# Kernel tuning notes

Hardware: AMD Instinct MI355X
Metric: run time of the kernel (lower is better)

The kernel has to match this reference:

```python
import math
import jax, jax.numpy as jnp
import numpy as np

B, H, S, D = 2, 16, 2048, 64


def setup_inputs() -> dict:
    key = jax.random.key(0)
    kq, kk, kv = jax.random.split(key, 3)
    query = jax.random.normal(kq, (B, H, S, D), dtype=jnp.float32)
    k = jax.random.normal(kk, (B, H, S, D), dtype=jnp.float32)
    value = jax.random.normal(kv, (B, H, S, D), dtype=jnp.float32)
    # causal mask: True = keep, broadcasts over batch and heads
    mask = jnp.tril(jnp.ones((S, S), dtype=bool))
    return {"query": query, "key": k, "value": value, "mask": mask}


def reference(query, key, value, mask):
    d_k = query.shape[-1]
    scale = 1.0 / math.sqrt(d_k)
    # (..., s1, s2) materialized scores, as in the original module
    scores = jnp.einsum("bhqd,bhkd->bhqk", query, key) * scale
    scores = jnp.where(mask, scores, -jnp.inf)
    # stable softmax = exp(x - max) / sum, same math as the torch softmax helper
    attn = jax.nn.softmax(scores, axis=-1)
    return jnp.einsum("bhqk,bhkd->bhqd", attn, value)
```

## Files before the change

### kernel.cpp

```cpp
#include <hip/hip_runtime.h>
#include <hip/hip_bf16.h>


typedef __attribute__((ext_vector_type(8))) short  s8v;
typedef __attribute__((ext_vector_type(4))) float  f4v;
typedef __attribute__((ext_vector_type(4))) unsigned int u4v;

#define SEQ 2048
#define DH  64
#define BHN 32
#define CSC 0.18033688f

#if __has_builtin(__builtin_amdgcn_exp2f)
#define EXP2(x) __builtin_amdgcn_exp2f(x)
#else
#define EXP2(x) exp2f(x)
#endif

__device__ __forceinline__ unsigned short f2bf(float x) {
  union { float f; unsigned int u; } v; v.f = x;
  return (unsigned short)((v.u + 0x7fffu + ((v.u >> 16) & 1u)) >> 16);
}
__device__ __forceinline__ float bf2f(unsigned short x) {
  union { unsigned int u; float f; } v; v.u = ((unsigned int)x) << 16;
  return v.f;
}
__device__ __forceinline__ int pack_bf2(float a, float b) {
  union { __hip_bfloat162 h; int i; } u;
  u.h = __float22bfloat162_rn(make_float2(a, b));
  return u.i;
}
__device__ __forceinline__ bool probe_is_f32(const unsigned short* p) {
  const unsigned e = (p[threadIdx.x & 63] >> 7) & 0xFFu;
  return __ballot(e >= 0x89u) != 0ULL;
}
__device__ __forceinline__ s8v cvt8(const float* p) {
  float4 a = *(const float4*)p;
  float4 b = *(const float4*)(p + 4);
  s8v r;
  r[0] = (short)f2bf(a.x); r[1] = (short)f2bf(a.y);
  r[2] = (short)f2bf(a.z); r[3] = (short)f2bf(a.w);
  r[4] = (short)f2bf(b.x); r[5] = (short)f2bf(b.y);
  r[6] = (short)f2bf(b.z); r[7] = (short)f2bf(b.w);
  return r;
}
__device__ __forceinline__ s8v cvt8s(const float* p, float s) {
  float4 a = *(const float4*)p;
  float4 b = *(const float4*)(p + 4);
  s8v r;
  r[0] = (short)f2bf(a.x * s); r[1] = (short)f2bf(a.y * s);
  r[2] = (short)f2bf(a.z * s); r[3] = (short)f2bf(a.w * s);
  r[4] = (short)f2bf(b.x * s); r[5] = (short)f2bf(b.y * s);
  r[6] = (short)f2bf(b.z * s); r[7] = (short)f2bf(b.w * s);
  return r;
}
__device__ __forceinline__ void gld16(const void* g, void* l) {
  __builtin_amdgcn_global_load_lds(
      (const __attribute__((address_space(1))) void*)g,
      (__attribute__((address_space(3))) void*)l, 16, 0, 0);
}

__global__ __launch_bounds__(256) void prep_kernel(
    const void* __restrict__ Kv, const void* __restrict__ Vv,
    unsigned short* __restrict__ Kbf, unsigned short* __restrict__ Vt) {
  const int bh = blockIdx.y;
  const int s0 = blockIdx.x * 64;
  const int t  = threadIdx.x;
  if (blockIdx.z == 0) {
    const unsigned short* K16 = (const unsigned short*)Kv;
    const float*          KF  = (const float*)Kv;
    const bool isF32 = probe_is_f32(K16);
    const int sr  = t >> 2;
    const int cb0 = (t & 3) * 32;
    const int xs  = (sr & 7) << 4;
    const size_t src = ((size_t)(bh * SEQ + s0 + sr)) * DH + (t & 3) * 16;
    s8v a0, a1;
    if (!isF32) { a0 = *(const s8v*)(K16 + src); a1 = *(const s8v*)(K16 + src + 8); }
    else        { a0 = cvt8(KF + src);           a1 = cvt8(KF + src + 8); }
    char* rowp = (char*)Kbf + ((size_t)(bh * SEQ + s0 + sr)) * 128;
    *(s8v*)(rowp + (cb0 ^ xs))        = a0;
    *(s8v*)(rowp + ((cb0 + 16) ^ xs)) = a1;
  } else {
    __shared__ __align__(16) unsigned short T[64][72];
    const unsigned short* V16 = (const unsigned short*)Vv;
    const float*          VF  = (const float*)Vv;
    const bool isF32 = probe_is_f32(V16);
    {
      const int sr = t >> 2, c0 = (t & 3) * 16;
      const size_t base = ((size_t)(bh * SEQ + s0 + sr)) * DH + c0;
      s8v a0, a1;
      if (!isF32) { a0 = *(const s8v*)(V16 + base); a1 = *(const s8v*)(V16 + base + 8); }
      else        { a0 = cvt8(VF + base);           a1 = cvt8(VF + base + 8); }
      *(s8v*)&T[sr][c0]     = a0;
      *(s8v*)&T[sr][c0 + 8] = a1;
    }
    __syncthreads();
    {
      const int d  = t & 63;
      const int hs = t >> 6;
      const int xs = (d & 7) << 4;
      char* rowp = (char*)Vt + (size_t)bh * SEQ * 128 + (size_t)s0 * 128
                 + (size_t)d * 128;
#pragma unroll
      for (int cc = 0; cc < 2; ++cc) {
        const int c  = hs * 2 + cc;
        const int kA = (c >> 2) * 32 + (c & 3) * 4;
        unsigned int wb[4];
        wb[0] = (unsigned int)T[kA + 0][d]  | ((unsigned int)T[kA + 1][d]  << 16);
        wb[1] = (unsigned int)T[kA + 2][d]  | ((unsigned int)T[kA + 3][d]  << 16);
        wb[2] = (unsigned int)T[kA + 16][d] | ((unsigned int)T[kA + 17][d] << 16);
        wb[3] = (unsigned int)T[kA + 18][d] | ((unsigned int)T[kA + 19][d] << 16);
        u4v q = { wb[0], wb[1], wb[2], wb[3] };
        *(u4v*)(rowp + ((c * 16) ^ xs)) = q;
      }
    }
  }
}

__global__ __launch_bounds__(128, 2) void attn_kernel(
    const void* __restrict__ Qv, const unsigned short* __restrict__ Kbf,
    const unsigned short* __restrict__ Vt, void* __restrict__ Outv) {
  __shared__ __align__(16) char Lds[2][16384];

  const unsigned short* Q16 = (const unsigned short*)Qv;
  const float*          QF  = (const float*)Qv;
  const bool isF32 = probe_is_f32(Q16);

  const int blk = blockIdx.x;
  const int bh  = (blk & 7) * 4 + ((blk >> 3) & 3);
  const int a   = (blk >> 5) & 7;
  const int bsl = blk >> 8;
  const int qb  = (bsl == 0) ? (7 - a) : (bsl == 1) ? (8 + a)
                : (bsl == 2) ? (23 - a) : (24 + a);

  const int tid  = threadIdx.x;
  const int w    = tid >> 6;
  const int lane = tid & 63;
  const int quad = lane >> 4;
  const int c16  = lane & 15;
  const int q0   = qb * 64 + w * 32;

  const size_t bh_off = (size_t)bh * SEQ * DH;

  s8v aq[2][2];
#pragma unroll
  for (int h = 0; h < 2; ++h)
#pragma unroll
    for (int kc = 0; kc < 2; ++kc) {
      const size_t idx = bh_off + (size_t)(q0 + h * 16 + c16) * DH + kc * 32 + quad * 8;
      if (isF32) aq[h][kc] = cvt8s(QF + idx, CSC);
      else {
        s8v aa = *(const s8v*)(Q16 + idx);
#pragma unroll
        for (int t = 0; t < 8; ++t)
          aa[t] = (short)f2bf(bf2f((unsigned short)aa[t]) * CSC);
        aq[h][kc] = aa;
      }
    }

  f4v o[2][4];
  float l[2] = {0.f, 0.f};
#pragma unroll
  for (int h = 0; h < 2; ++h)
#pragma unroll
    for (int i = 0; i < 4; ++i) { f4v z = {0.f, 0.f, 0.f, 0.f}; o[h][i] = z; }

  const int ntiles = qb + 1;

  const int xorl = (c16 & 7) << 4;
  const int fc0  = (quad * 16) ^ xorl;
  const int fc1  = (64 + quad * 16) ^ xorl;
  const int frow = c16 * 128;

  const unsigned short* Kg = Kbf + bh_off + (size_t)lane * 8;
  const unsigned short* Vg = Vt  + bh_off + (size_t)lane * 8;

  auto stage = [&](int tile, int buf) {
    if (w == 0) {
      const unsigned short* g = Kg + (size_t)tile * 4096;
      char* lp = &Lds[buf][0];
#pragma unroll
      for (int j = 0; j < 8; ++j) gld16(g + j * 512, lp + j * 1024);
    } else {
      const unsigned short* g = Vg + (size_t)tile * 4096;
      char* lp = &Lds[buf][8192];
#pragma unroll
      for (int j = 0; j < 8; ++j) gld16(g + j * 512, lp + j * 1024);
    }
  };

  stage(0, 0);
  __syncthreads();

  for (int kt = 0; kt < ntiles; ++kt) {
    const int cb = kt & 1, nb = cb ^ 1;
    if (kt + 1 < ntiles) stage(kt + 1, nb);

    const char* Kl = &Lds[cb][0];
    const char* Vl = &Lds[cb][8192];
    s8v kb[4][2], vb[4][2];
#pragma unroll
    for (int nt = 0; nt < 4; ++nt) {
      kb[nt][0] = *(const s8v*)(Kl + frow + nt * 2048 + fc0);
      kb[nt][1] = *(const s8v*)(Kl + frow + nt * 2048 + fc1);
      vb[nt][0] = *(const s8v*)(Vl + frow + nt * 2048 + fc0);
      vb[nt][1] = *(const s8v*)(Vl + frow + nt * 2048 + fc1);
    }

    __builtin_amdgcn_s_setprio(1);
    float p[2][4][4];
#pragma unroll
    for (int h = 0; h < 2; ++h)
#pragma unroll
      for (int nt = 0; nt < 4; ++nt) {
        f4v acc = {0.f, 0.f, 0.f, 0.f};
        acc = __builtin_amdgcn_mfma_f32_16x16x32_bf16(kb[nt][0], aq[h][0], acc, 0, 0, 0);
        acc = __builtin_amdgcn_mfma_f32_16x16x32_bf16(kb[nt][1], aq[h][1], acc, 0, 0, 0);
#pragma unroll
        for (int r = 0; r < 4; ++r) p[h][nt][r] = EXP2(acc[r]);
      }
    if (kt * 64 + 63 > q0) {
#pragma unroll
      for (int h = 0; h < 2; ++h) {
        const int qmk = q0 + h * 16 + c16 - kt * 64 - quad * 4;
#pragma unroll
        for (int nt = 0; nt < 4; ++nt)
#pragma unroll
          for (int r = 0; r < 4; ++r)
            if (nt * 16 + r > qmk) p[h][nt][r] = 0.f;
      }
    }
#pragma unroll
    for (int h = 0; h < 2; ++h) {
      float s = 0.f;
#pragma unroll
      for (int nt = 0; nt < 4; ++nt)
        s += (p[h][nt][0] + p[h][nt][1]) + (p[h][nt][2] + p[h][nt][3]);
      l[h] += s;
#pragma unroll
      for (int kc = 0; kc < 2; ++kc) {
        union { int d[4]; s8v v; } u;
        u.d[0] = pack_bf2(p[h][2 * kc][0],     p[h][2 * kc][1]);
        u.d[1] = pack_bf2(p[h][2 * kc][2],     p[h][2 * kc][3]);
        u.d[2] = pack_bf2(p[h][2 * kc + 1][0], p[h][2 * kc + 1][1]);
        u.d[3] = pack_bf2(p[h][2 * kc + 1][2], p[h][2 * kc + 1][3]);
#pragma unroll
        for (int dt = 0; dt < 4; ++dt)
          o[h][dt] = __builtin_amdgcn_mfma_f32_16x16x32_bf16(u.v, vb[dt][kc], o[h][dt], 0, 0, 0);
      }
    }
    __builtin_amdgcn_s_setprio(0);

    __syncthreads();
  }

#pragma unroll
  for (int h = 0; h < 2; ++h) {
    float lv = l[h];
    lv += __shfl_xor(lv, 16);
    lv += __shfl_xor(lv, 32);
    union { float f; int i; } lu; lu.f = lv;
    float invr[4];
#pragma unroll
    for (int rr = 0; rr < 4; ++rr) {
      union { int i; float f; } tf;
      tf.i = __builtin_amdgcn_ds_bpermute(4 * (quad * 4 + rr), lu.i);
      invr[rr] = 1.0f / tf.f;
    }
    if (isF32) {
      float* OF = (float*)Outv;
#pragma unroll
      for (int rr = 0; rr < 4; ++rr) {
        const size_t rb = bh_off + (size_t)(q0 + h * 16 + quad * 4 + rr) * DH + c16;
#pragma unroll
        for (int dt = 0; dt < 4; ++dt)
          OF[rb + dt * 16] = o[h][dt][rr] * invr[rr];
      }
    } else {
      unsigned short* O16 = (unsigned short*)Outv;
#pragma unroll
      for (int rr = 0; rr < 4; ++rr) {
        const size_t rb = bh_off + (size_t)(q0 + h * 16 + quad * 4 + rr) * DH + c16;
#pragma unroll
        for (int dt = 0; dt < 4; ++dt)
          O16[rb + dt * 16] = f2bf(o[h][dt][rr] * invr[rr]);
      }
    }
  }
}

extern "C" void kernel_launch(void* const* d_in, const int* in_sizes, int n_in,
                              void* d_out, int out_size, void* d_ws, size_t ws_size,
                              hipStream_t stream) {
  const void* Q = d_in[0];
  const void* K = d_in[1];
  const void* V = d_in[2];
  unsigned short* Kbf = (unsigned short*)d_ws;
  unsigned short* Vt  = Kbf + (size_t)BHN * SEQ * DH;

  dim3 g1(SEQ / 64, BHN, 2);
  prep_kernel<<<g1, 256, 0, stream>>>(K, V, Kbf, Vt);
  attn_kernel<<<dim3(1024), 128, 0, stream>>>(Q, Kbf, Vt, d_out);
}
```

Before: 138.5 us.

## Split KV tiles across waves with per-wave pipelines and LDS merge

Rather than two waves each owning 32 query rows and sharing one KV tile per iteration, each wave now handles all 64 query rows and takes alternate KV tiles. Each wave runs its own double-buffered LDS pipeline with explicit vmcnt/lgkmcnt waits, so the per-tile __syncthreads is gone. The two partial outputs and row sums are merged through LDS at the end. Block ordering becomes a plain largest-first order. The cost is twice the accumulator registers, 64KB of LDS per block (which may limit occupancy), and possible imbalance when the tile count is odd.

Result: slower. 154.0 us (+11.2%).

```diff
diff --git a/kernel.cpp b/kernel.cpp
--- a/kernel.cpp
+++ b/kernel.cpp
@@ -120,7 +120,7 @@
 __global__ __launch_bounds__(128, 2) void attn_kernel(
     const void* __restrict__ Qv, const unsigned short* __restrict__ Kbf,
     const unsigned short* __restrict__ Vt, void* __restrict__ Outv) {
-  __shared__ __align__(16) char Lds[2][16384];
+  __shared__ __align__(16) char Lds[65536];
 
   const unsigned short* Q16 = (const unsigned short*)Qv;
   const float*          QF  = (const float*)Qv;
@@ -128,23 +128,23 @@
 
   const int blk = blockIdx.x;
   const int bh  = (blk & 7) * 4 + ((blk >> 3) & 3);
-  const int a   = (blk >> 5) & 7;
-  const int bsl = blk >> 8;
-  const int qb  = (bsl == 0) ? (7 - a) : (bsl == 1) ? (8 + a)
-                : (bsl == 2) ? (23 - a) : (24 + a);
+  const int qb  = 31 - (blk >> 5);
 
   const int tid  = threadIdx.x;
   const int w    = tid >> 6;
   const int lane = tid & 63;
   const int quad = lane >> 4;
   const int c16  = lane & 15;
-  const int q0   = qb * 64 + w * 32;
+  const int q0   = qb * 64;
+
+  const int ntiles = qb + 1;
+  const int nw = (ntiles - w + 1) >> 1;
 
   const size_t bh_off = (size_t)bh * SEQ * DH;
 
-  s8v aq[2][2];
-#pragma unroll
-  for (int h = 0; h < 2; ++h)
+  s8v aq[4][2];
+#pragma unroll
+  for (int h = 0; h < 4; ++h)
 #pragma unroll
     for (int kc = 0; kc < 2; ++kc) {
       const size_t idx = bh_off + (size_t)(q0 + h * 16 + c16) * DH + kc * 32 + quad * 8;
@@ -158,14 +158,12 @@
       }
     }
 
-  f4v o[2][4];
-  float l[2] = {0.f, 0.f};
-#pragma unroll
-  for (int h = 0; h < 2; ++h)
+  f4v o[4][4];
+  float l[4] = {0.f, 0.f, 0.f, 0.f};
+#pragma unroll
+  for (int h = 0; h < 4; ++h)
 #pragma unroll
     for (int i = 0; i < 4; ++i) { f4v z = {0.f, 0.f, 0.f, 0.f}; o[h][i] = z; }
-
-  const int ntiles = qb + 1;
 
   const int xorl = (c16 & 7) << 4;
   const int fc0  = (quad * 16) ^ xorl;
@@ -175,115 +173,153 @@
   const unsigned short* Kg = Kbf + bh_off + (size_t)lane * 8;
   const unsigned short* Vg = Vt  + bh_off + (size_t)lane * 8;
 
+  char* LdsW = &Lds[w * 32768];
+
   auto stage = [&](int tile, int buf) {
-    if (w == 0) {
-      const unsigned short* g = Kg + (size_t)tile * 4096;
-      char* lp = &Lds[buf][0];
-#pragma unroll
-      for (int j = 0; j < 8; ++j) gld16(g + j * 512, lp + j * 1024);
+    const unsigned short* gk = Kg + (size_t)tile * 4096;
+    const unsigned short* gv = Vg + (size_t)tile * 4096;
+    char* lk = LdsW + buf * 16384;
+    char* lv = lk + 8192;
+#pragma unroll
+    for (int j = 0; j < 8; ++j) gld16(gk + j * 512, lk + j * 1024);
+#pragma unroll
+    for (int j = 0; j < 8; ++j) gld16(gv + j * 512, lv + j * 1024);
+  };
+
+  if (nw > 0) {
+    stage(w, 0);
+    if (nw > 1) {
+      stage(w + 2, 1);
+      asm volatile("s_waitcnt vmcnt(16)" ::: "memory");
     } else {
-      const unsigned short* g = Vg + (size_t)tile * 4096;
-      char* lp = &Lds[buf][8192];
-#pragma unroll
-      for (int j = 0; j < 8; ++j) gld16(g + j * 512, lp + j * 1024);
-    }
-  };
-
-  stage(0, 0);
-  __syncthreads();
-
-  for (int kt = 0; kt < ntiles; ++kt) {
-    const int cb = kt & 1, nb = cb ^ 1;
-    if (kt + 1 < ntiles) stage(kt + 1, nb);
-
-    const char* Kl = &Lds[cb][0];
-    const char* Vl = &Lds[cb][8192];
-    s8v kb[4][2], vb[4][2];
-#pragma unroll
-    for (int nt = 0; nt < 4; ++nt) {
-      kb[nt][0] = *(const s8v*)(Kl + frow + nt * 2048 + fc0);
-      kb[nt][1] = *(const s8v*)(Kl + frow + nt * 2048 + fc1);
-      vb[nt][0] = *(const s8v*)(Vl + frow + nt * 2048 + fc0);
-      vb[nt][1] = *(const s8v*)(Vl + frow + nt * 2048 + fc1);
-    }
-
-    __builtin_amdgcn_s_setprio(1);
-    float p[2][4][4];
-#pragma unroll
-    for (int h = 0; h < 2; ++h)
+      asm volatile("s_waitcnt vmcnt(0)" ::: "memory");
+    }
+    __builtin_amdgcn_sched_barrier(0);
+
+    for (int j = 0; j < nw; ++j) {
+      const int kt = w + 2 * j;
+      const int cb = j & 1;
+
+      const char* Kl = LdsW + cb * 16384;
+      const char* Vl = Kl + 8192;
+      s8v kb[4][2], vb[4][2];
 #pragma unroll
       for (int nt = 0; nt < 4; ++nt) {
-        f4v acc = {0.f, 0.f, 0.f, 0.f};
-        acc = __builtin_amdgcn_mfma_f32_16x16x32_bf16(kb[nt][0], aq[h][0], acc, 0, 0, 0);
-        acc = __builtin_amdgcn_mfma_f32_16x16x32_bf16(kb[nt][1], aq[h][1], acc, 0, 0, 0);
-#pragma unroll
-        for (int r = 0; r < 4; ++r) p[h][nt][r] = EXP2(acc[r]);
-      }
-    if (kt * 64 + 63 > q0) {
-#pragma unroll
-      for (int h = 0; h < 2; ++h) {
-        const int qmk = q0 + h * 16 + c16 - kt * 64 - quad * 4;
+        kb[nt][0] = *(const s8v*)(Kl + frow + nt * 2048 + fc0);
+        kb[nt][1] = *(const s8v*)(Kl + frow + nt * 2048 + fc1);
+        vb[nt][0] = *(const s8v*)(Vl + frow + nt * 2048 + fc0);
+        vb[nt][1] = *(const s8v*)(Vl + frow + nt * 2048 + fc1);
+      }
+      asm volatile("s_waitcnt lgkmcnt(0)" ::: "memory");
+      __builtin_amdgcn_sched_barrier(0);
+
+      if (j + 2 < nw) stage(w + 2 * (j + 2), cb);
+
+      const bool diag = (kt == qb);
+      __builtin_amdgcn_s_setprio(1);
+#pragma unroll
+      for (int h = 0; h < 4; ++h) {
+        float p[4][4];
+#pragma unroll
+        for (int nt = 0; nt < 4; ++nt) {
+          f4v acc = {0.f, 0.f, 0.f, 0.f};
+          acc = __builtin_amdgcn_mfma_f32_16x16x32_bf16(kb[nt][0], aq[h][0], acc, 0, 0, 0);
+          acc = __builtin_amdgcn_mfma_f32_16x16x32_bf16(kb[nt][1], aq[h][1], acc, 0, 0, 0);
+#pragma unroll
+          for (int r = 0; r < 4; ++r) p[nt][r] = EXP2(acc[r]);
+        }
+        if (diag) {
+          const int qmk = q0 + h * 16 + c16 - kt * 64 - quad * 4;
+#pragma unroll
+          for (int nt = 0; nt < 4; ++nt)
+#pragma unroll
+            for (int r = 0; r < 4; ++r)
+              if (nt * 16 + r > qmk) p[nt][r] = 0.f;
+        }
+        float s = 0.f;
 #pragma unroll
         for (int nt = 0; nt < 4; ++nt)
-#pragma unroll
-          for (int r = 0; r < 4; ++r)
-            if (nt * 16 + r > qmk) p[h][nt][r] = 0.f;
-      }
-    }
-#pragma unroll
-    for (int h = 0; h < 2; ++h) {
-      float s = 0.f;
-#pragma unroll
-      for (int nt = 0; nt < 4; ++nt)
-        s += (p[h][nt][0] + p[h][nt][1]) + (p[h][nt][2] + p[h][nt][3]);
-      l[h] += s;
-#pragma unroll
-      for (int kc = 0; kc < 2; ++kc) {
-        union { int d[4]; s8v v; } u;
-        u.d[0] = pack_bf2(p[h][2 * kc][0],     p[h][2 * kc][1]);
-        u.d[1] = pack_bf2(p[h][2 * kc][2],     p[h][2 * kc][3]);
-        u.d[2] = pack_bf2(p[h][2 * kc + 1][0], p[h][2 * kc + 1][1]);
-        u.d[3] = pack_bf2(p[h][2 * kc + 1][2], p[h][2 * kc + 1][3]);
-#pragma unroll
-        for (int dt = 0; dt < 4; ++dt)
-          o[h][dt] = __builtin_amdgcn_mfma_f32_16x16x32_bf16(u.v, vb[dt][kc], o[h][dt], 0, 0, 0);
-      }
-    }
-    __builtin_amdgcn_s_setprio(0);
-
-    __syncthreads();
-  }
-
-#pragma unroll
-  for (int h = 0; h < 2; ++h) {
+          s += (p[nt][0] + p[nt][1]) + (p[nt][2] + p[nt][3]);
+        l[h] += s;
+#pragma unroll
+        for (int kc = 0; kc < 2; ++kc) {
+          union { int d[4]; s8v v; } u;
+          u.d[0] = pack_bf2(p[2 * kc][0],     p[2 * kc][1]);
+          u.d[1] = pack_bf2(p[2 * kc][2],     p[2 * kc][3]);
+          u.d[2] = pack_bf2(p[2 * kc + 1][0], p[2 * kc + 1][1]);
+          u.d[3] = pack_bf2(p[2 * kc + 1][2], p[2 * kc + 1][3]);
+#pragma unroll
+          for (int dt = 0; dt < 4; ++dt)
+            o[h][dt] = __builtin_amdgcn_mfma_f32_16x16x32_bf16(u.v, vb[dt][kc], o[h][dt], 0, 0, 0);
+        }
+      }
+      __builtin_amdgcn_s_setprio(0);
+
+      if (j + 1 < nw) {
+        if (j + 2 < nw) asm volatile("s_waitcnt vmcnt(16)" ::: "memory");
+        else            asm volatile("s_waitcnt vmcnt(0)"  ::: "memory");
+        __builtin_amdgcn_sched_barrier(0);
+      }
+    }
+  }
+
+  f4v lpack;
+#pragma unroll
+  for (int h = 0; h < 4; ++h) {
     float lv = l[h];
     lv += __shfl_xor(lv, 16);
     lv += __shfl_xor(lv, 32);
-    union { float f; int i; } lu; lu.f = lv;
-    float invr[4];
-#pragma unroll
-    for (int rr = 0; rr < 4; ++rr) {
-      union { int i; float f; } tf;
-      tf.i = __builtin_amdgcn_ds_bpermute(4 * (quad * 4 + rr), lu.i);
-      invr[rr] = 1.0f / tf.f;
-    }
-    if (isF32) {
-      float* OF = (float*)Outv;
+    lpack[h] = lv;
+  }
+  {
+    char* C = LdsW;
+#pragma unroll
+    for (int h = 0; h < 4; ++h)
+#pragma unroll
+      for (int dt = 0; dt < 4; ++dt)
+        *(f4v*)(C + lane * 256 + (h * 4 + dt) * 16) = o[h][dt];
+    *(f4v*)(C + 16384 + lane * 16) = lpack;
+  }
+  __syncthreads();
+  {
+    const char* P = &Lds[(1 - w) * 32768];
+    const f4v pl = *(const f4v*)(P + 16384 + lane * 16);
+#pragma unroll
+    for (int hh = 0; hh < 2; ++hh) {
+      const int h = 2 * w + hh;
+      const float ltot = lpack[h] + pl[h];
+      union { float f; int i; } lu; lu.f = ltot;
+      float invr[4];
 #pragma unroll
       for (int rr = 0; rr < 4; ++rr) {
-        const size_t rb = bh_off + (size_t)(q0 + h * 16 + quad * 4 + rr) * DH + c16;
-#pragma unroll
-        for (int dt = 0; dt < 4; ++dt)
-          OF[rb + dt * 16] = o[h][dt][rr] * invr[rr];
-      }
-    } else {
-      unsigned short* O16 = (unsigned short*)Outv;
-#pragma unroll
-      for (int rr = 0; rr < 4; ++rr) {
-        const size_t rb = bh_off + (size_t)(q0 + h * 16 + quad * 4 + rr) * DH + c16;
-#pragma unroll
-        for (int dt = 0; dt < 4; ++dt)
-          O16[rb + dt * 16] = f2bf(o[h][dt][rr] * invr[rr]);
+        union { int i; float f; } tf;
+        tf.i = __builtin_amdgcn_ds_bpermute(4 * (quad * 4 + rr), lu.i);
+        invr[rr] = 1.0f / tf.f;
+      }
+      f4v ot[4];
+#pragma unroll
+      for (int dt = 0; dt < 4; ++dt) {
+        const f4v po = *(const f4v*)(P + lane * 256 + (h * 4 + dt) * 16);
+        ot[dt] = o[h][dt] + po;
+      }
+      if (isF32) {
+        float* OF = (float*)Outv;
+#pragma unroll
+        for (int rr = 0; rr < 4; ++rr) {
+          const size_t rb = bh_off + (size_t)(q0 + h * 16 + quad * 4 + rr) * DH + c16;
+#pragma unroll
+          for (int dt = 0; dt < 4; ++dt)
+            OF[rb + dt * 16] = ot[dt][rr] * invr[rr];
+        }
+      } else {
+        unsigned short* O16 = (unsigned short*)Outv;
+#pragma unroll
+        for (int rr = 0; rr < 4; ++rr) {
+          const size_t rb = bh_off + (size_t)(q0 + h * 16 + quad * 4 + rr) * DH + c16;
+#pragma unroll
+          for (int dt = 0; dt < 4; ++dt)
+            O16[rb + dt * 16] = f2bf(ot[dt][rr] * invr[rr]);
+        }
       }
     }
   }
```
